# Optimization experiments

Hardware: AMD Instinct MI355X
Metric: run time of the kernel (lower is better)

## Reference

```python
import jax, jax.numpy as jnp
import numpy as np

_PROFILE = [2, 3, 4]  # direction exponents per scale -> 4, 8, 16 directions


def _make_filter_banks():
    """Build per-scale grouped-conv filter banks.
    Returns list of arrays [3*num_dirs, 1, k, k] (same filters tiled for R,G,B groups)."""
    banks = []
    for scale, exp in enumerate(_PROFILE):
        num_dirs = 2 ** exp
        size = 11 + 4 * scale
        center = size // 2
        coords = np.arange(size) - center
        X, Y = np.meshgrid(coords, coords)
        kernels = []
        for d in range(num_dirs):
            angle = np.pi * d / num_dirs
            Xr = X * np.cos(angle) + Y * np.sin(angle)
            Yr = -X * np.sin(angle) + Y * np.cos(angle)
            freq = 0.3 / 2 ** scale
            dir_bandwidth = 2.0
            env = np.exp(-(Xr ** 2 + (dir_bandwidth * Yr) ** 2) / (2 * (size / 4) ** 2))
            k = env * np.cos(2 * np.pi * freq * Xr)
            k = k / (np.abs(k).sum() + 1e-8)
            kernels.append(k)
        bank = np.stack(kernels)[:, None]          # [nd, 1, k, k]
        bank = np.tile(bank, (3, 1, 1, 1))          # [3*nd, 1, k, k] (groups = RGB)
        banks.append(jnp.asarray(bank, dtype=jnp.float32))
    return banks


def setup_inputs() -> dict:
    key = jax.random.key(0)
    rgb_image = jax.random.normal(key, (4, 3, 512, 512), dtype=jnp.float32)
    f0, f1, f2 = _make_filter_banks()
    return {"rgb_image": rgb_image, "f0": f0, "f1": f1, "f2": f2}


def _grouped_conv(x, w):
    # x: [B,3,H,W], w: [3*nd,1,k,k]; SAME padding (k odd), one group per RGB channel.
    p = w.shape[-1] // 2
    return jax.lax.conv_general_dilated(
        x, w, window_strides=(1, 1), padding=[(p, p), (p, p)],
        feature_group_count=3,
        dimension_numbers=("NCHW", "OIHW", "NCHW"))


def reference(rgb_image, f0, f1, f2):
    B, C, H, W = rgb_image.shape
    # Directional subbands per scale, grouped by channel: [B, 3, nd, H, W]
    s0 = _grouped_conv(rgb_image, f0).reshape(B, 3, 4, H, W)
    s1 = _grouped_conv(rgb_image, f1).reshape(B, 3, 8, H, W)
    s2 = _grouped_conv(rgb_image, f2).reshape(B, 3, 16, H, W)
    # Low-frequency branch: avg_pool2d(k=4,s=4) then bilinear upsample (align_corners=False)
    low = rgb_image.reshape(B, 3, H // 4, 4, W // 4, 4).mean(axis=(3, 5))
    low = jax.image.resize(low, (B, 3, H, W), method="linear")
    low = low[:, :, None]  # [B, 3, 1, H, W]
    # Per channel: [s0 dirs, s1 dirs, s2 dirs, low] -> 29 bands; 3 channels -> 87
    out = jnp.concatenate([s0, s1, s2, low], axis=2).reshape(B, 87, H, W)
    return out
```

## Files before the change

### kernel.cpp

```cpp
#include <hip/hip_runtime.h>
#include <hip/hip_bf16.h>

#define HW 512

typedef __attribute__((ext_vector_type(8))) short bf16x8;
typedef __attribute__((ext_vector_type(4))) float floatx4;

union BFrag { uint2 u2[2]; bf16x8 v; };

static __device__ inline ushort f2bf(float f) {
    __hip_bfloat16 h = __float2bfloat16(f);
    return *(ushort*)&h;
}

template<int K, int NDIR, int SUB0, int YPACK, int OCTS, int NSTEP>
__global__ __launch_bounds__(256)
void mfma_conv(const float* __restrict__ img, const float* __restrict__ filt,
               float* __restrict__ out)
{
    constexpr int R       = K / 2;
    constexpr int TILE_W  = 64, TILE_H = 32;
    constexpr int NCHAIN  = TILE_H / YPACK;
    constexpr int ROWSP   = (4 * NSTEP - 1) / OCTS + 1;
    constexpr int EXT_Y   = (TILE_H - YPACK) + ROWSP;
    constexpr int EXT_X   = 4 * 15 + 8 * (OCTS - 1) + 8;
    constexpr int SPX     = (EXT_X + 7) & ~7;
    constexpr int P       = (OCTS == 3) ? 3 : 1;
    constexpr int GSTRIDE = (4 * P / OCTS) * SPX;

    __shared__ __align__(16) ushort s_img[EXT_Y * SPX];

    const int tid   = threadIdx.x;
    const int bx    = blockIdx.x, by = blockIdx.y, plane = blockIdx.z;
    const int bb    = plane / 3, cc = plane % 3;
    const float* __restrict__ src = img + (size_t)plane * HW * HW;
    const int gx0 = bx * TILE_W, gy0 = by * TILE_H;

    constexpr int PAIRS = SPX / 2;
    for (int idx = tid; idx < EXT_Y * PAIRS; idx += 256) {
        const int row = idx / PAIRS;
        const int col = (idx - row * PAIRS) * 2;
        const int gy = gy0 - R + row;
        const int gx = gx0 - R + col;
        float v0 = 0.f, v1 = 0.f;
        if ((unsigned)gy < HW) {
            if ((unsigned)gx       < HW) v0 = src[gy * HW + gx];
            if ((unsigned)(gx + 1) < HW) v1 = src[gy * HW + gx + 1];
        }
        *(uint*)&s_img[row * SPX + col] = ((uint)f2bf(v1) << 16) | (uint)f2bf(v0);
    }

    const int lane = tid & 63;
    const int r    = tid >> 6;
    const int mn   = lane & 15;
    const int q    = lane >> 4;
    const int dirm = mn & (NDIR - 1);
    const int yoffm = mn / NDIR;

    bf16x8 afrag[NSTEP];
    #pragma unroll
    for (int s = 0; s < NSTEP; ++s) {
        #pragma unroll
        for (int j = 0; j < 8; ++j) {
            const int c   = 4 * s + q;
            const int dyu = c / OCTS, o = c - dyu * OCTS;
            const int dy  = dyu - yoffm;
            const int dx  = 8 * o + j - r;
            float fv = 0.f;
            if (dy >= 0 && dy < K && dx >= 0 && dx < K)
                fv = filt[(dirm * K + dy) * K + dx];
            afrag[s][j] = (short)f2bf(fv);
        }
    }
    __syncthreads();

    int base0[P];
    #pragma unroll
    for (int s0 = 0; s0 < P; ++s0) {
        const int c0   = 4 * s0 + q;
        const int dyu0 = c0 / OCTS, o0 = c0 - dyu0 * OCTS;
        base0[s0] = dyu0 * SPX + 8 * o0 + 4 * mn;
    }

    const int px = gx0 + r + 4 * mn;

    for (int ch = 0; ch < NCHAIN; ++ch) {
        const int y = ch * YPACK;
        floatx4 acc = {0.f, 0.f, 0.f, 0.f};
        #pragma unroll
        for (int s = 0; s < NSTEP; ++s) {
            const int s0 = s % P, g = s / P;
            const ushort* p = s_img + (base0[s0] + y * SPX + g * GSTRIDE);
            BFrag b;
            b.u2[0] = *(const uint2*)p;
            b.u2[1] = *(const uint2*)(p + 4);
            acc = __builtin_amdgcn_mfma_f32_16x16x32_bf16(afrag[s], b.v, acc, 0, 0, 0);
        }
        #pragma unroll
        for (int i = 0; i < 4; ++i) {
            const int mrow = q * 4 + i;
            const int dd = mrow & (NDIR - 1);
            const int yo = mrow / NDIR;
            const int Y  = gy0 + y + yo;
            out[((size_t)(bb * 87 + cc * 29 + SUB0 + dd) * HW + Y) * HW + px] = acc[i];
        }
    }
}

__global__ __launch_bounds__(256)
void low_kernel(const float* __restrict__ img, float* __restrict__ out)
{
    __shared__ float s_p[34 * 35];
    const int tid   = threadIdx.x;
    const int bx    = blockIdx.x, by = blockIdx.y;
    const int plane = blockIdx.z;
    const int b     = plane / 3, c = plane % 3;
    const float* __restrict__ src = img + (size_t)plane * HW * HW;
    const int lx0 = bx * 32, ly0 = by * 32;

    for (int idx = tid; idx < 34 * 34; idx += 256) {
        const int r = idx / 34, col = idx % 34;
        const int ly = min(max(ly0 - 1 + r,   0), 127);
        const int lx = min(max(lx0 - 1 + col, 0), 127);
        const float* p = src + (size_t)(ly * 4) * HW + lx * 4;
        float s = 0.f;
        #pragma unroll
        for (int rr = 0; rr < 4; ++rr) {
            const float4 v = *(const float4*)(p + (size_t)rr * HW);
            s += v.x + v.y + v.z + v.w;
        }
        s_p[r * 35 + col] = s * (1.f / 16.f);
    }
    __syncthreads();

    const size_t outbase = (size_t)(b * 87 + c * 29 + 28) * HW * HW;
    for (int k = 0; k < 64; ++k) {
        const int pix = tid + k * 256;
        const int ry = pix >> 7, rx = pix & 127;
        const int gy = ly0 * 4 + ry, gx = lx0 * 4 + rx;
        const float cy = (gy - 1.5f) * 0.25f;
        const float cx = (gx - 1.5f) * 0.25f;
        const int jy = (int)floorf(cy), jx = (int)floorf(cx);
        const float fy = cy - jy, fx = cx - jx;
        const int tyy = jy - (ly0 - 1);
        const int txx = jx - (lx0 - 1);
        const float p00 = s_p[tyy * 35 + txx],       p01 = s_p[tyy * 35 + txx + 1];
        const float p10 = s_p[(tyy + 1) * 35 + txx], p11 = s_p[(tyy + 1) * 35 + txx + 1];
        const float v0 = p00 + fx * (p01 - p00);
        const float v1 = p10 + fx * (p11 - p10);
        out[outbase + (size_t)gy * HW + gx] = v0 + fy * (v1 - v0);
    }
}

extern "C" void kernel_launch(void* const* d_in, const int* in_sizes, int n_in,
                              void* d_out, int out_size, void* d_ws, size_t ws_size,
                              hipStream_t stream)
{
    const float* img = (const float*)d_in[0];
    const float* f0  = (const float*)d_in[1];
    const float* f1  = (const float*)d_in[2];
    const float* f2  = (const float*)d_in[3];
    float* out = (float*)d_out;

    dim3 block(256);
    dim3 grid(HW / 64, HW / 32, 12);

    mfma_conv<11,  4,  0, 4, 2,  7><<<grid, block, 0, stream>>>(img, f0, out);
    mfma_conv<15,  8,  4, 2, 3, 12><<<grid, block, 0, stream>>>(img, f1, out);
    mfma_conv<19, 16, 12, 1, 3, 15><<<grid, block, 0, stream>>>(img, f2, out);
    low_kernel<<<dim3(4, 4, 12), block, 0, stream>>>(img, out);
}
```

Before: 538.6 us.

## Switch to 32x32x16 MFMA, wider tiles, fused scale kernel with precomputed A fragments

Replaces the three per-scale 16x16x32 MFMA conv kernels with a single fused launch that dispatches by scale on blockIdx.z. It uses 32x32x16 bf16 MFMA over 128-wide tiles and processes four chains per pass to reuse each A fragment. The filter A-fragments are now built once by a small prep kernel into a global buffer and streamed from memory, instead of being recomputed in registers by every block. This is meant to cut per-block filter setup and raise MFMA throughput per LDS load. In exchange it adds an extra launch, more accumulator registers (occupancy hint 4) and global loads of A inside the inner loop.

```diff
diff --git a/kernel.cpp b/kernel.cpp
--- a/kernel.cpp
+++ b/kernel.cpp
@@ -4,7 +4,7 @@
 #define HW 512
 
 typedef __attribute__((ext_vector_type(8))) short bf16x8;
-typedef __attribute__((ext_vector_type(4))) float floatx4;
+typedef __attribute__((ext_vector_type(16))) float floatx16;
 
 union BFrag { uint2 u2[2]; bf16x8 v; };
 
@@ -13,25 +13,32 @@
     return *(ushort*)&h;
 }
 
-template<int K, int NDIR, int SUB0, int YPACK, int OCTS, int NSTEP>
-__global__ __launch_bounds__(256)
-void mfma_conv(const float* __restrict__ img, const float* __restrict__ filt,
-               float* __restrict__ out)
-{
+__device__ __align__(16) short g_afrag[(18 + 27 + 30) * 256 * 8];
+
+template<int K, int NDIR, int SUB0, int OCTS, int NSTEP, int AOFF>
+__device__ __forceinline__
+void conv_body(ushort* __restrict__ s_img,
+               const float* __restrict__ img, float* __restrict__ out,
+               const int plane)
+{
+    constexpr int YPACK   = 32 / NDIR;
     constexpr int R       = K / 2;
-    constexpr int TILE_W  = 64, TILE_H = 32;
+    constexpr int TILE_W  = 128, TILE_H = 32;
     constexpr int NCHAIN  = TILE_H / YPACK;
-    constexpr int ROWSP   = (4 * NSTEP - 1) / OCTS + 1;
-    constexpr int EXT_Y   = (TILE_H - YPACK) + ROWSP;
-    constexpr int EXT_X   = 4 * 15 + 8 * (OCTS - 1) + 8;
+    constexpr int CB      = 4;
+    constexpr int NPASS   = NCHAIN / CB;
+    constexpr int ROWS_A  = K + YPACK - 1;
+    constexpr int EXT_Y   = (TILE_H - YPACK) + ROWS_A;
+    constexpr int EXT_X   = 4 * 31 + 8 * (OCTS - 1) + 8;
     constexpr int SPX     = (EXT_X + 7) & ~7;
     constexpr int P       = (OCTS == 3) ? 3 : 1;
-    constexpr int GSTRIDE = (4 * P / OCTS) * SPX;
-
-    __shared__ __align__(16) ushort s_img[EXT_Y * SPX];
+    constexpr int GSTRIDE = (2 * P / OCTS) * SPX;
+    constexpr int NG      = NSTEP / P;
+    static_assert(NSTEP % P == 0, "octet chunking must be exact");
+    static_assert(NSTEP * 2 == ROWS_A * OCTS, "step count must cover octets");
 
     const int tid   = threadIdx.x;
-    const int bx    = blockIdx.x, by = blockIdx.y, plane = blockIdx.z;
+    const int bx    = blockIdx.x, by = blockIdx.y;
     const int bb    = plane / 3, cc = plane % 3;
     const float* __restrict__ src = img + (size_t)plane * HW * HW;
     const int gx0 = bx * TILE_W, gy0 = by * TILE_H;
@@ -49,62 +56,109 @@
         }
         *(uint*)&s_img[row * SPX + col] = ((uint)f2bf(v1) << 16) | (uint)f2bf(v0);
     }
+    __syncthreads();
 
     const int lane = tid & 63;
     const int r    = tid >> 6;
-    const int mn   = lane & 15;
-    const int q    = lane >> 4;
-    const int dirm = mn & (NDIR - 1);
-    const int yoffm = mn / NDIR;
-
-    bf16x8 afrag[NSTEP];
+    const int n    = lane & 31;
+    const int h    = lane >> 5;
+
+    int base0[P];
     #pragma unroll
+    for (int s0 = 0; s0 < P; ++s0) {
+        const int c0   = 2 * s0 + h;
+        const int dyu0 = c0 / OCTS, o0 = c0 - dyu0 * OCTS;
+        base0[s0] = dyu0 * SPX + 8 * o0 + 4 * n;
+    }
+
+    const int px = gx0 + r + 4 * n;
+    const short* __restrict__ abase = g_afrag + ((size_t)AOFF + tid) * 8;
+
+    for (int p = 0; p < NPASS; ++p) {
+        floatx16 acc[CB] = {};
+        const ushort* bp = s_img + p * (CB * YPACK * SPX);
+        const short*  ap = abase;
+        for (int gi = 0; gi < NG; ++gi) {
+            #pragma unroll
+            for (int s0 = 0; s0 < P; ++s0) {
+                const bf16x8 a = *(const bf16x8*)(ap + s0 * 256 * 8);
+                #pragma unroll
+                for (int i = 0; i < CB; ++i) {
+                    const ushort* q = bp + (base0[s0] + i * (YPACK * SPX));
+                    BFrag b;
+                    b.u2[0] = *(const uint2*)q;
+                    b.u2[1] = *(const uint2*)(q + 4);
+                    acc[i] = __builtin_amdgcn_mfma_f32_32x32x16_bf16(a, b.v, acc[i], 0, 0, 0);
+                }
+            }
+            bp += GSTRIDE;
+            ap += P * 256 * 8;
+        }
+        #pragma unroll
+        for (int i = 0; i < CB; ++i) {
+            #pragma unroll
+            for (int reg = 0; reg < 16; ++reg) {
+                const int m  = (reg & 3) + 8 * (reg >> 2) + 4 * h;
+                const int dd = m & (NDIR - 1);
+                const int yo = m / NDIR;
+                const int Y  = gy0 + (p * CB + i) * YPACK + yo;
+                out[((size_t)(bb * 87 + cc * 29 + SUB0 + dd) * HW + Y) * HW + px] = acc[i][reg];
+            }
+        }
+    }
+}
+
+#define SMEM_ELEMS 7600
+
+__global__ __launch_bounds__(256, 4)
+void fused_conv(const float* __restrict__ img, float* __restrict__ out)
+{
+    __shared__ __align__(16) ushort s_img[SMEM_ELEMS];
+    const int z  = blockIdx.z;
+    const int sc = z % 3;
+    const int plane = z / 3;
+    if (sc == 0) {
+        conv_body<19, 16, 12, 3, 30, (18 + 27) * 256>(s_img, img, out, plane);
+    } else if (sc == 1) {
+        conv_body<15,  8,  4, 3, 27, 18 * 256>(s_img, img, out, plane);
+    } else {
+        conv_body<11,  4,  0, 2, 18, 0>(s_img, img, out, plane);
+    }
+}
+
+template<int K, int NDIR, int OCTS, int NSTEP, int AOFF>
+__device__ __forceinline__
+void prep_body(const float* __restrict__ filt)
+{
+    const int tid  = threadIdx.x;
+    const int lane = tid & 63, r = tid >> 6;
+    const int m    = lane & 31, h = lane >> 5;
+    const int dirm  = m & (NDIR - 1);
+    const int yoffm = m / NDIR;
     for (int s = 0; s < NSTEP; ++s) {
+        bf16x8 v;
         #pragma unroll
         for (int j = 0; j < 8; ++j) {
-            const int c   = 4 * s + q;
+            const int c   = 2 * s + h;
             const int dyu = c / OCTS, o = c - dyu * OCTS;
             const int dy  = dyu - yoffm;
             const int dx  = 8 * o + j - r;
             float fv = 0.f;
             if (dy >= 0 && dy < K && dx >= 0 && dx < K)
                 fv = filt[(dirm * K + dy) * K + dx];
-            afrag[s][j] = (short)f2bf(fv);
-        }
-    }
-    __syncthreads();
-
-    int base0[P];
-    #pragma unroll
-    for (int s0 = 0; s0 < P; ++s0) {
-        const int c0   = 4 * s0 + q;
-        const int dyu0 = c0 / OCTS, o0 = c0 - dyu0 * OCTS;
-        base0[s0] = dyu0 * SPX + 8 * o0 + 4 * mn;
-    }
-
-    const int px = gx0 + r + 4 * mn;
-
-    for (int ch = 0; ch < NCHAIN; ++ch) {
-        const int y = ch * YPACK;
-        floatx4 acc = {0.f, 0.f, 0.f, 0.f};
-        #pragma unroll
-        for (int s = 0; s < NSTEP; ++s) {
-            const int s0 = s % P, g = s / P;
-            const ushort* p = s_img + (base0[s0] + y * SPX + g * GSTRIDE);
-            BFrag b;
-            b.u2[0] = *(const uint2*)p;
-            b.u2[1] = *(const uint2*)(p + 4);
-            acc = __builtin_amdgcn_mfma_f32_16x16x32_bf16(afrag[s], b.v, acc, 0, 0, 0);
-        }
-        #pragma unroll
-        for (int i = 0; i < 4; ++i) {
-            const int mrow = q * 4 + i;
-            const int dd = mrow & (NDIR - 1);
-            const int yo = mrow / NDIR;
-            const int Y  = gy0 + y + yo;
-            out[((size_t)(bb * 87 + cc * 29 + SUB0 + dd) * HW + Y) * HW + px] = acc[i];
-        }
-    }
+            v[j] = (short)f2bf(fv);
+        }
+        *(bf16x8*)&g_afrag[((size_t)AOFF + s * 256 + tid) * 8] = v;
+    }
+}
+
+__global__ __launch_bounds__(256)
+void prep_afrag(const float* __restrict__ f0, const float* __restrict__ f1,
+                const float* __restrict__ f2)
+{
+    if (blockIdx.x == 0)      prep_body<11,  4, 2, 18, 0>(f0);
+    else if (blockIdx.x == 1) prep_body<15,  8, 3, 27, 18 * 256>(f1);
+    else                      prep_body<19, 16, 3, 30, (18 + 27) * 256>(f2);
 }
 
 __global__ __launch_bounds__(256)
@@ -163,10 +217,7 @@
     float* out = (float*)d_out;
 
     dim3 block(256);
-    dim3 grid(HW / 64, HW / 32, 12);
-
-    mfma_conv<11,  4,  0, 4, 2,  7><<<grid, block, 0, stream>>>(img, f0, out);
-    mfma_conv<15,  8,  4, 2, 3, 12><<<grid, block, 0, stream>>>(img, f1, out);
-    mfma_conv<19, 16, 12, 1, 3, 15><<<grid, block, 0, stream>>>(img, f2, out);
+    prep_afrag<<<dim3(3), block, 0, stream>>>(f0, f1, f2);
+    fused_conv<<<dim3(HW / 128, HW / 32, 36), block, 0, stream>>>(img, out);
     low_kernel<<<dim3(4, 4, 12), block, 0, stream>>>(img, out);
 }
```

After: 563.0 us. 4.5% more time.
